# Kernel optimization log

Measured on AMD Instinct MI355X. Metric: run time of the kernel, lower is better.

The kernel has to match this reference:

```python
import jax, jax.numpy as jnp
import numpy as np

DIM = 96
NUM_EXPERTS = 4
TOP_K = 1

def setup_inputs() -> dict:
    key = jax.random.key(0)
    ks = jax.random.split(key, 8)
    B, C, H, W = 16, DIM, 128, 128
    E = NUM_EXPERTS
    x = jax.random.normal(ks[0], (B, C, H, W), dtype=jnp.float32)
    # per-expert depthwise 3x3 conv (groups=C): torch weight [C,1,3,3]
    dw_w = jax.random.normal(ks[1], (E, C, 1, 3, 3), dtype=jnp.float32) * 0.1
    dw_b = jax.random.normal(ks[2], (E, C), dtype=jnp.float32) * 0.05
    # per-expert pointwise 1x1 conv: torch weight [C,C,1,1]
    pw_w = jax.random.normal(ks[3], (E, C, C, 1, 1), dtype=jnp.float32) * 0.1
    pw_b = jax.random.normal(ks[4], (E, C), dtype=jnp.float32) * 0.05
    # router linear: torch weight [E, C]
    router_w = jax.random.normal(ks[5], (E, C), dtype=jnp.float32) * 0.1
    router_b = jax.random.normal(ks[6], (E,), dtype=jnp.float32) * 0.05
    return {"x": x, "dw_w": dw_w, "dw_b": dw_b, "pw_w": pw_w, "pw_b": pw_b,
            "router_w": router_w, "router_b": router_b}

def _conv(x, w, groups):
    return jax.lax.conv_general_dilated(
        x, w, window_strides=(1, 1), padding='SAME',
        dimension_numbers=('NCHW', 'OIHW', 'NCHW'),
        feature_group_count=groups)

def _expert(x, dw_w, dw_b, pw_w, pw_b):
    C = x.shape[1]
    h = _conv(x, dw_w, groups=C) + dw_b[None, :, None, None]   # depthwise 3x3
    h = jax.nn.gelu(h, approximate=False)                       # torch GELU (erf)
    return _conv(h, pw_w, groups=1) + pw_b[None, :, None, None] # 1x1 conv

def reference(x, dw_w, dw_b, pw_w, pw_b, router_w, router_b):
    B, C, H, W = x.shape
    E = dw_w.shape[0]
    # router: global avg pool -> linear -> softmax
    pooled = jnp.mean(x, axis=(2, 3))                            # [B, C]
    logits = pooled @ router_w.T + router_b                      # [B, E]
    router_weights = jax.nn.softmax(logits, axis=-1)
    top_weights, top_indices = jax.lax.top_k(router_weights, TOP_K)  # [B, k]
    top_weights = top_weights / (jnp.sum(top_weights, axis=-1, keepdims=True) + 1e-8)
    # run all experts (faithful to the original, which does not dispatch)
    expert_outputs = jnp.stack(
        [_expert(x, dw_w[e], dw_b[e], pw_w[e], pw_b[e]) for e in range(E)],
        axis=1)                                                  # [B, E, C, H, W]
    # scatter top-k weights into dense gates [B, E]
    gates = jnp.zeros((B, E), dtype=x.dtype)
    gates = gates.at[jnp.arange(B)[:, None], top_indices].set(top_weights)
    return jnp.einsum('bechw,be->bchw', expert_outputs, gates)
```

## Files before the change

### kernel.cpp

```cpp
#include <hip/hip_runtime.h>
#include <math.h>

#define DIM 96
#define NE 4
#define HH 128
#define WW 128
#define BB 16
#define KP 24
#define HSROW (KP * 2)
#define HSBUF (WW * HSROW)
#define PWROW 192

typedef __attribute__((ext_vector_type(8))) __bf16 bf16x8;
typedef __attribute__((ext_vector_type(4))) float floatx4;

__device__ __forceinline__ unsigned short f2bf(float f) {
    unsigned u = __builtin_bit_cast(unsigned, f);
    unsigned r = u + 0x7FFFu + ((u >> 16) & 1u);
    return (unsigned short)(r >> 16);
}
__device__ __forceinline__ unsigned pack2(float a, float b) {
    return (unsigned)f2bf(a) | ((unsigned)f2bf(b) << 16);
}

__device__ __forceinline__ float dpp_up1(float v) {
    return __builtin_bit_cast(float, __builtin_amdgcn_mov_dpp(
        __builtin_bit_cast(int, v), 0x138, 0xF, 0xF, true));
}
__device__ __forceinline__ float dpp_down1(float v) {
    return __builtin_bit_cast(float, __builtin_amdgcn_mov_dpp(
        __builtin_bit_cast(int, v), 0x130, 0xF, 0xF, true));
}

__device__ __forceinline__ void barrier_lds_only() {
    asm volatile("s_waitcnt lgkmcnt(0)" ::: "memory");
    __builtin_amdgcn_s_barrier();
}

__device__ __forceinline__ float gelu_erf(float h) {
    const float x = h * 0.70710678118654752f;
    const float a = fabsf(x);
    const float t = __builtin_amdgcn_rcpf(__builtin_fmaf(0.3275911f, a, 1.0f));
    float p = __builtin_fmaf(1.061405429f, t, -1.453152027f);
    p = __builtin_fmaf(p, t, 1.421413741f);
    p = __builtin_fmaf(p, t, -0.284496736f);
    p = __builtin_fmaf(p, t, 0.254829592f);
    p *= t;
    const float e = __expf(-x * x);
    float erfv = __builtin_fmaf(-p, e, 1.0f);
    erfv = copysignf(erfv, x);
    return 0.5f * h * (1.0f + erfv);
}

__global__ __launch_bounds__(256) void pool_kernel(const float* __restrict__ x,
                                                   float* __restrict__ pooled) {
    const int bc = blockIdx.x;
    const float4* p = (const float4*)(x + (size_t)bc * (HH * WW));
    const int t = threadIdx.x;
    float s = 0.f;
#pragma unroll
    for (int k = 0; k < (HH * WW / 4) / 256; ++k) {
        float4 v = p[t + k * 256];
        s += v.x + v.y + v.z + v.w;
    }
#pragma unroll
    for (int off = 32; off; off >>= 1) s += __shfl_down(s, off, 64);
    __shared__ float ls[4];
    if ((t & 63) == 0) ls[t >> 6] = s;
    __syncthreads();
    if (t == 0) pooled[bc] = (ls[0] + ls[1] + ls[2] + ls[3]) * (1.0f / (HH * WW));
}

__device__ __forceinline__ void issue_sub(const float* __restrict__ x, int b,
                                          int cbase, int cg, int rr0, int r,
                                          int rr2, int p4, float4 f[2][3]) {
#pragma unroll
    for (int u = 0; u < 2; ++u) {
        const float* pl = x + (size_t)(b * DIM + cbase + cg * 2 + u) * (HH * WW);
        f[u][0] = *(const float4*)(pl + rr0 * WW + p4);
        f[u][1] = *(const float4*)(pl + r   * WW + p4);
        f[u][2] = *(const float4*)(pl + rr2 * WW + p4);
    }
}

__device__ __forceinline__ void compute_sub(const float4 f[2][3],
                                            const float (*dwc)[12], int cb,
                                            int cg, float lmask, float rmask,
                                            unsigned char* hsbuf, int p4,
                                            unsigned swz) {
    float hq[2][4];
#pragma unroll
    for (int u = 0; u < 2; ++u) {
        const int c = cb + cg * 2 + u;
        const float4 wA = *(const float4*)&dwc[c][0];
        const float4 wB = *(const float4*)&dwc[c][4];
        const float4 wC = *(const float4*)&dwc[c][8];
        float h0 = wC.y, h1 = wC.y, h2 = wC.y, h3 = wC.y;
#pragma unroll
        for (int row = 0; row < 3; ++row) {
            const float ta = (row == 0) ? wA.x : ((row == 1) ? wA.w : wB.z);
            const float tb = (row == 0) ? wA.y : ((row == 1) ? wB.x : wB.w);
            const float tc = (row == 0) ? wA.z : ((row == 1) ? wB.y : wC.x);
            const float4 f4 = f[u][row];
            const float vl = dpp_up1(f4.w) * lmask;
            const float vr = dpp_down1(f4.x) * rmask;
            h0 = __builtin_fmaf(ta, vl,   __builtin_fmaf(tb, f4.x, __builtin_fmaf(tc, f4.y, h0)));
            h1 = __builtin_fmaf(ta, f4.x, __builtin_fmaf(tb, f4.y, __builtin_fmaf(tc, f4.z, h1)));
            h2 = __builtin_fmaf(ta, f4.y, __builtin_fmaf(tb, f4.z, __builtin_fmaf(tc, f4.w, h2)));
            h3 = __builtin_fmaf(ta, f4.z, __builtin_fmaf(tb, f4.w, __builtin_fmaf(tc, vr, h3)));
        }
        hq[u][0] = gelu_erf(h0);
        hq[u][1] = gelu_erf(h1);
        hq[u][2] = gelu_erf(h2);
        hq[u][3] = gelu_erf(h3);
    }
    const unsigned wb0 = (unsigned)(p4 * HSROW + cg * 4);
#pragma unroll
    for (int j = 0; j < 4; ++j) {
        const unsigned off = (wb0 + (unsigned)j * HSROW) ^ swz;
        *(unsigned*)(hsbuf + off) = pack2(hq[0][j], hq[1][j]);
    }
}

__global__ __launch_bounds__(256, 3) void moe_main(
    const float* __restrict__ x, const float* __restrict__ dw_w,
    const float* __restrict__ dw_b, const float* __restrict__ pw_w,
    const float* __restrict__ pw_b, const float* __restrict__ pooled,
    const float* __restrict__ rw, const float* __restrict__ rb,
    float* __restrict__ out) {
    __shared__ __align__(16) unsigned char pwb[DIM * PWROW];
    __shared__ __align__(16) unsigned char hsb[4 * HSBUF];
    __shared__ float dwc[DIM][12];
    __shared__ float lsm[4];

    const int t = threadIdx.x;
    const unsigned bid = blockIdx.x;
    const int xcd = bid & 7;
    const int s = bid >> 3;
    const int b = xcd * 2 + (s >> 7);
    const int r = s & 127;

    const int lane = t & 63, w = t >> 6;
    const int wm = w & 1, wn = w >> 1;
    const int ln = lane & 15, kg = lane >> 4;
    const int cobase = wm * 48, pxbase = wn * 64;

    const int g32 = t & 31;
    const int p4 = g32 * 4;
    const int cg = t >> 5;
    const unsigned swz = (unsigned)((g32 & 7) << 4);
    const float lmask = (p4 == 0) ? 0.f : 1.f;
    const float rmask = (p4 == 124) ? 0.f : 1.f;

    const float m0 = (r > 0) ? 1.f : 0.f;
    const float m2 = (r < HH - 1) ? 1.f : 0.f;
    const int rr0 = (r > 0) ? r - 1 : 0;
    const int rr2 = (r < HH - 1) ? r + 1 : HH - 1;

    float4 fA[2][3], fB[2][3];
    issue_sub(x, b, 0, cg, rr0, r, rr2, p4, fA);
    issue_sub(x, b, 16, cg, rr0, r, rr2, p4, fB);

    {
        float part = pooled[b * DIM + lane] * rw[w * DIM + lane];
        if (lane < 32)
            part += pooled[b * DIM + 64 + lane] * rw[w * DIM + 64 + lane];
#pragma unroll
        for (int off = 32; off; off >>= 1) part += __shfl_down(part, off, 64);
        if (lane == 0) lsm[w] = part + rb[w];
    }
    barrier_lds_only();
    int e;
    float g;
    {
        const float l0 = lsm[0], l1 = lsm[1], l2 = lsm[2], l3 = lsm[3];
        float m = l0; int mi = 0;
        if (l1 > m) { m = l1; mi = 1; }
        if (l2 > m) { m = l2; mi = 2; }
        if (l3 > m) { m = l3; mi = 3; }
        const float denom = __expf(l0 - m) + __expf(l1 - m) +
                            __expf(l2 - m) + __expf(l3 - m);
        const float wv = 1.0f / denom;
        g = wv / (wv + 1e-8f);
        e = mi;
    }

#pragma unroll
    for (int i = 0; i < 18; ++i) {
        const int u = i * 256 + t;
        const int co = u / 48, kp = u - co * 48;
        const float2 v = *(const float2*)(pw_w +
            ((size_t)e * DIM + co) * DIM + kp * 2);
        *(unsigned*)(pwb + ((unsigned)(co * PWROW + kp * 4) ^
                            (unsigned)((co & 7) << 4))) = pack2(v.x, v.y);
    }
    for (int j = t; j < DIM * 12; j += 256) {
        const int c = j / 12, q = j - c * 12;
        float v = 0.f;
        if (q < 9) {
            v = dw_w[((size_t)e * DIM + c) * 9 + q];
            if (q < 3) v *= m0;
            if (q >= 6) v *= m2;
        } else if (q == 9) v = dw_b[e * DIM + c];
        dwc[c][q] = v;
    }
    barrier_lds_only();

    bf16x8 af[3][3];
#pragma unroll
    for (int pair = 0; pair < 3; ++pair)
#pragma unroll
        for (int mf = 0; mf < 3; ++mf) {
            const int co = cobase + mf * 16 + ln;
            af[pair][mf] = *(const bf16x8*)(pwb +
                ((unsigned)(co * PWROW + pair * 64 + kg * 16) ^
                 (unsigned)((co & 7) << 4)));
        }

    floatx4 acc[3][4];
#pragma unroll
    for (int i = 0; i < 3; ++i)
#pragma unroll
        for (int j = 0; j < 4; ++j) acc[i][j] = (floatx4){0.f, 0.f, 0.f, 0.f};

#pragma unroll
    for (int pair = 0; pair < 3; ++pair) {
        const int cb = pair * 32;
        unsigned char* h0 = hsb + (unsigned)((pair & 1) * 2) * HSBUF;
        unsigned char* h1 = h0 + HSBUF;
        compute_sub(fA, dwc, cb, cg, lmask, rmask, h0, p4, swz);
        if (pair < 2) issue_sub(x, b, cb + 32, cg, rr0, r, rr2, p4, fA);
        compute_sub(fB, dwc, cb + 16, cg, lmask, rmask, h1, p4, swz);
        if (pair < 2) issue_sub(x, b, cb + 48, cg, rr0, r, rr2, p4, fB);
        barrier_lds_only();

        const unsigned qbase = (unsigned)((pair & 1) * 2 + (kg >> 1)) * HSBUF;
        bf16x8 bfr[4];
#pragma unroll
        for (int nf = 0; nf < 4; ++nf) {
            const int pxv = pxbase + nf * 16 + ln;
            const unsigned boff = (unsigned)((pxv * HSROW + (kg & 1) * 16) ^
                                             (((pxv >> 2) & 7) << 4));
            bfr[nf] = *(const bf16x8*)(hsb + qbase + boff);
        }
#pragma unroll
        for (int mf = 0; mf < 3; ++mf)
#pragma unroll
            for (int nf = 0; nf < 4; ++nf)
                acc[mf][nf] = __builtin_amdgcn_mfma_f32_16x16x32_bf16(
                    af[pair][mf], bfr[nf], acc[mf][nf], 0, 0, 0);
    }

#pragma unroll
    for (int mf = 0; mf < 3; ++mf) {
#pragma unroll
        for (int rr = 0; rr < 4; ++rr) {
            const int co = cobase + mf * 16 + kg * 4 + rr;
            const float bias = pw_b[e * DIM + co];
            float* orow = out + ((size_t)(b * DIM + co) * HH + r) * WW;
#pragma unroll
            for (int nf = 0; nf < 4; ++nf)
                orow[pxbase + nf * 16 + ln] = (acc[mf][nf][rr] + bias) * g;
        }
    }
}

extern "C" void kernel_launch(void* const* d_in, const int* in_sizes, int n_in,
                              void* d_out, int out_size, void* d_ws, size_t ws_size,
                              hipStream_t stream) {
    const float* x    = (const float*)d_in[0];
    const float* dw_w = (const float*)d_in[1];
    const float* dw_b = (const float*)d_in[2];
    const float* pw_w = (const float*)d_in[3];
    const float* pw_b = (const float*)d_in[4];
    const float* rw   = (const float*)d_in[5];
    const float* rb   = (const float*)d_in[6];
    float* out = (float*)d_out;

    float* pooled = (float*)d_ws;

    pool_kernel<<<BB * DIM, 256, 0, stream>>>(x, pooled);
    moe_main<<<HH * BB, 256, 0, stream>>>(x, dw_w, dw_b, pw_w, pw_b,
                                          pooled, rw, rb, out);
}
```

Before: 67.72 us.

## Load pointwise weights per-pair from global into registers, drop LDS staging

Removes the shared-memory staging buffer for the bf16 pointwise weights. Each pair of K-chunks now loads its A fragments straight from global memory as fp32 and converts them to bf16 in registers just before the MFMAs. This frees about 18KB of LDS and cuts live A-fragment registers from 9 to 3, and the launch bound is raised to 4 blocks per CU. The cost is redundant global/L2 weight reads per block and per-pair conversion work.

```diff
diff --git a/kernel.cpp b/kernel.cpp
--- a/kernel.cpp
+++ b/kernel.cpp
@@ -9,7 +9,6 @@
 #define KP 24
 #define HSROW (KP * 2)
 #define HSBUF (WW * HSROW)
-#define PWROW 192
 
 typedef __attribute__((ext_vector_type(8))) __bf16 bf16x8;
 typedef __attribute__((ext_vector_type(4))) float floatx4;
@@ -122,13 +121,12 @@
     }
 }
 
-__global__ __launch_bounds__(256, 3) void moe_main(
+__global__ __launch_bounds__(256, 4) void moe_main(
     const float* __restrict__ x, const float* __restrict__ dw_w,
     const float* __restrict__ dw_b, const float* __restrict__ pw_w,
     const float* __restrict__ pw_b, const float* __restrict__ pooled,
     const float* __restrict__ rw, const float* __restrict__ rb,
     float* __restrict__ out) {
-    __shared__ __align__(16) unsigned char pwb[DIM * PWROW];
     __shared__ __align__(16) unsigned char hsb[4 * HSBUF];
     __shared__ float dwc[DIM][12];
     __shared__ float lsm[4];
@@ -185,15 +183,6 @@
         e = mi;
     }
 
-#pragma unroll
-    for (int i = 0; i < 18; ++i) {
-        const int u = i * 256 + t;
-        const int co = u / 48, kp = u - co * 48;
-        const float2 v = *(const float2*)(pw_w +
-            ((size_t)e * DIM + co) * DIM + kp * 2);
-        *(unsigned*)(pwb + ((unsigned)(co * PWROW + kp * 4) ^
-                            (unsigned)((co & 7) << 4))) = pack2(v.x, v.y);
-    }
     for (int j = t; j < DIM * 12; j += 256) {
         const int c = j / 12, q = j - c * 12;
         float v = 0.f;
@@ -206,17 +195,6 @@
     }
     barrier_lds_only();
 
-    bf16x8 af[3][3];
-#pragma unroll
-    for (int pair = 0; pair < 3; ++pair)
-#pragma unroll
-        for (int mf = 0; mf < 3; ++mf) {
-            const int co = cobase + mf * 16 + ln;
-            af[pair][mf] = *(const bf16x8*)(pwb +
-                ((unsigned)(co * PWROW + pair * 64 + kg * 16) ^
-                 (unsigned)((co & 7) << 4)));
-        }
-
     floatx4 acc[3][4];
 #pragma unroll
     for (int i = 0; i < 3; ++i)
@@ -228,12 +206,30 @@
         const int cb = pair * 32;
         unsigned char* h0 = hsb + (unsigned)((pair & 1) * 2) * HSBUF;
         unsigned char* h1 = h0 + HSBUF;
+        float4 a0[3], a1[3];
+#pragma unroll
+        for (int mf = 0; mf < 3; ++mf) {
+            const float* ap = pw_w + ((size_t)e * DIM + cobase + mf * 16 + ln) * DIM
+                              + cb + kg * 8;
+            a0[mf] = *(const float4*)ap;
+            a1[mf] = *(const float4*)(ap + 4);
+        }
         compute_sub(fA, dwc, cb, cg, lmask, rmask, h0, p4, swz);
         if (pair < 2) issue_sub(x, b, cb + 32, cg, rr0, r, rr2, p4, fA);
         compute_sub(fB, dwc, cb + 16, cg, lmask, rmask, h1, p4, swz);
         if (pair < 2) issue_sub(x, b, cb + 48, cg, rr0, r, rr2, p4, fB);
         barrier_lds_only();
 
+        bf16x8 af[3];
+#pragma unroll
+        for (int mf = 0; mf < 3; ++mf) {
+            uint4 u;
+            u.x = pack2(a0[mf].x, a0[mf].y);
+            u.y = pack2(a0[mf].z, a0[mf].w);
+            u.z = pack2(a1[mf].x, a1[mf].y);
+            u.w = pack2(a1[mf].z, a1[mf].w);
+            af[mf] = __builtin_bit_cast(bf16x8, u);
+        }
         const unsigned qbase = (unsigned)((pair & 1) * 2 + (kg >> 1)) * HSBUF;
         bf16x8 bfr[4];
 #pragma unroll
@@ -248,7 +244,7 @@
 #pragma unroll
             for (int nf = 0; nf < 4; ++nf)
                 acc[mf][nf] = __builtin_amdgcn_mfma_f32_16x16x32_bf16(
-                    af[pair][mf], bfr[nf], acc[mf][nf], 0, 0, 0);
+                    af[mf], bfr[nf], acc[mf][nf], 0, 0, 0);
     }
 
 #pragma unroll
```

After: 84.56 us. 24.9% more time.
